# Kernel tuning notes

Hardware: AMD Instinct MI355X
Metric: run time of the kernel (lower is better)

## Reference

```python
import jax, jax.numpy as jnp
import numpy as np

EPS = 1e-5

def _conv(x, w, pad, groups=1):
    return jax.lax.conv_general_dilated(
        x, w, window_strides=(1, 1), padding=[(pad, pad), (pad, pad)],
        dimension_numbers=('NCHW', 'OIHW', 'NCHW'), feature_group_count=groups)

def _bn(x, g, b, m, v):
    # inference batch-norm, per-channel
    s = g * jax.lax.rsqrt(v + EPS)
    return x * s[None, :, None, None] + (b - m * s)[None, :, None, None]

def setup_inputs() -> dict:
    key = jax.random.key(0)
    ks = jax.random.split(key, 20)
    B, C, H, W = 32, 128, 64, 64
    cs = C // 2  # c_split = 64
    d = {
        'x': jax.random.normal(ks[0], (B, C, H, W), jnp.float32),
        'weights': jax.random.uniform(ks[1], (B, 2), jnp.float32),
        'indices': jax.random.randint(ks[2], (B, 2), 0, 4, jnp.int32),
        # expert 0: Conv(cs -> C, k=3, p=1) + BN + SiLU
        'e0_w': jax.random.normal(ks[3], (C, cs, 3, 3), jnp.float32) * 0.05,
        'e0_g': jax.random.uniform(ks[4], (C,), jnp.float32, 0.5, 1.5),
        'e0_b': jax.random.normal(ks[5], (C,), jnp.float32) * 0.1,
        'e0_m': jax.random.normal(ks[6], (C,), jnp.float32) * 0.1,
        'e0_v': jax.random.uniform(ks[7], (C,), jnp.float32, 0.5, 1.5),
        # expert 1: depthwise 5x5 (cs, groups=cs) -> 1x1 (cs -> C) -> BN -> SiLU
        'e1_dw': jax.random.normal(ks[8], (cs, 1, 5, 5), jnp.float32) * 0.05,
        'e1_pw': jax.random.normal(ks[9], (C, cs, 1, 1), jnp.float32) * 0.05,
        'e1_g': jax.random.uniform(ks[10], (C,), jnp.float32, 0.5, 1.5),
        'e1_b': jax.random.normal(ks[11], (C,), jnp.float32) * 0.1,
        'e1_m': jax.random.normal(ks[12], (C,), jnp.float32) * 0.1,
        'e1_v': jax.random.uniform(ks[13], (C,), jnp.float32, 0.5, 1.5),
        # expert 2: GhostConv(C -> C): cv1 = Conv(C, C//2, 3), cv2 = Conv(C//2, C//2, 5, groups=C//2)
        'e2a_w': jax.random.normal(ks[14], (cs, C, 3, 3), jnp.float32) * 0.05,
        'e2a_g': jax.random.uniform(ks[15], (cs,), jnp.float32, 0.5, 1.5),
        'e2a_b': jax.random.normal(ks[16], (cs,), jnp.float32) * 0.1,
        'e2a_m': jax.random.normal(ks[17], (cs,), jnp.float32) * 0.1,
        'e2a_v': jax.random.uniform(ks[18], (cs,), jnp.float32, 0.5, 1.5),
        'e2b_w': jax.random.normal(ks[19], (cs, 1, 5, 5), jnp.float32) * 0.05,
    }
    ks2 = jax.random.split(jax.random.key(1), 4)
    d['e2b_g'] = jax.random.uniform(ks2[0], (cs,), jnp.float32, 0.5, 1.5)
    d['e2b_b'] = jax.random.normal(ks2[1], (cs,), jnp.float32) * 0.1
    d['e2b_m'] = jax.random.normal(ks2[2], (cs,), jnp.float32) * 0.1
    d['e2b_v'] = jax.random.uniform(ks2[3], (cs,), jnp.float32, 0.5, 1.5)
    return d

def _forward(x, weights, indices,
             e0_w, e0_g, e0_b, e0_m, e0_v,
             e1_dw, e1_pw, e1_g, e1_b, e1_m, e1_v,
             e2a_w, e2a_g, e2a_b, e2a_m, e2a_v,
             e2b_w, e2b_g, e2b_b, e2b_m, e2b_v):
    C = x.shape[1]
    cs = C // 2
    x_rgb, x_ir = x[:, :cs], x[:, cs:]
    # expert outputs computed densely over the whole batch, masked combine below
    e0 = jax.nn.silu(_bn(_conv(x_rgb, e0_w, pad=1), e0_g, e0_b, e0_m, e0_v))
    e1 = jax.nn.silu(_bn(_conv(_conv(x_ir, e1_dw, pad=2, groups=cs), e1_pw, pad=0),
                         e1_g, e1_b, e1_m, e1_v))
    g1 = jax.nn.silu(_bn(_conv(x, e2a_w, pad=1), e2a_g, e2a_b, e2a_m, e2a_v))
    g2 = jax.nn.silu(_bn(_conv(g1, e2b_w, pad=2, groups=cs), e2b_g, e2b_b, e2b_m, e2b_v))
    e2 = jnp.concatenate([g1, g2], axis=1)
    out = jnp.zeros_like(x)
    K = indices.shape[1]
    for k in range(K):  # small fixed top-k loop
        idx = indices[:, k][:, None, None, None]          # [B,1,1,1]
        w = weights[:, k][:, None, None, None]            # [B,1,1,1]
        out = out + jnp.where(idx == 0, e0 * w, 0.0)
        out = out + jnp.where(idx == 1, e1 * w, 0.0)
        out = out + jnp.where(idx == 2, e2 * w, 0.0)
        out = out + jnp.where(idx == 3, x * 0.1, 0.0)
    return out

def reference(x, weights, indices,
              e0_w, e0_g, e0_b, e0_m, e0_v,
              e1_dw, e1_pw, e1_g, e1_b, e1_m, e1_v,
              e2a_w, e2a_g, e2a_b, e2a_m, e2a_v,
              e2b_w, e2b_g, e2b_b, e2b_m, e2b_v):
    return _forward(x, weights, indices,
                    e0_w, e0_g, e0_b, e0_m, e0_v,
                    e1_dw, e1_pw, e1_g, e1_b, e1_m, e1_v,
                    e2a_w, e2a_g, e2a_b, e2a_m, e2a_v,
                    e2b_w, e2b_g, e2b_b, e2b_m, e2b_v)
```

## Files before the change

kernel.cpp:

```cpp
#include <hip/hip_runtime.h>

#define B_  32
#define C_  128
#define CS  64
#define H_  64
#define W_  64
#define HW  (H_*W_)

typedef __attribute__((ext_vector_type(8))) short bf16x8_t;
typedef __attribute__((ext_vector_type(4))) float f32x4_t;
typedef unsigned short u16;
typedef unsigned int   u32;

__device__ __forceinline__ float silu_f(float v) { return v / (1.f + __expf(-v)); }

__device__ __forceinline__ u16 f2bf(float f) {
    u32 u = __float_as_uint(f);
    u = (u + 0x7FFFu + ((u >> 16) & 1u)) >> 16;
    return (u16)u;
}
__device__ __forceinline__ float bf2f(u16 u) {
    return __uint_as_float(((u32)u) << 16);
}
__device__ __forceinline__ u32 cvtpk(float a, float b) {
    u32 r;
    asm("v_cvt_pk_bf16_f32 %0, %1, %2" : "=v"(r) : "v"(a), "v"(b));
    return r;
}

__device__ __forceinline__ void get_coeffs(const float* __restrict__ wts,
                                           const int* __restrict__ idxs, int b,
                                           float& c0, float& c1, float& c2, float& cid) {
    int   i0 = idxs[b*2+0], i1 = idxs[b*2+1];
    float w0 = wts[b*2+0],  w1 = wts[b*2+1];
    c0  = (i0==0?w0:0.f)   + (i1==0?w1:0.f);
    c1  = (i0==1?w0:0.f)   + (i1==1?w1:0.f);
    c2  = (i0==2?w0:0.f)   + (i1==2?w1:0.f);
    cid = (i0==3?0.1f:0.f) + (i1==3?0.1f:0.f);
}

__global__ __launch_bounds__(256) void k_prep(
    const float* __restrict__ e0w, const float* __restrict__ e2aw, const float* __restrict__ e1pw,
    u16* __restrict__ Wt0f, u16* __restrict__ Wt2f, u16* __restrict__ Wt1f)
{
    const int i0 = blockIdx.x*256 + threadIdx.x, stride = gridDim.x*256;
    for (int i = i0; i < 73728; i += stride) {
        int j = i&7, lane = (i>>3)&63, cog = (i>>9)&7, kc = (i>>12)&1, tap = i>>13;
        int co = cog*16 + (lane&15), ci = kc*32 + (lane>>4)*8 + j;
        Wt0f[i] = f2bf(e0w[(size_t)(co*64 + ci)*9 + tap]);
    }
    for (int i = i0; i < 73728; i += stride) {
        int j = i&7, lane = (i>>3)&63, cog = (i>>9)&3, kc = (i>>11)&3, tap = i>>13;
        int co = cog*16 + (lane&15), ci = kc*32 + (lane>>4)*8 + j;
        Wt2f[i] = f2bf(e2aw[(size_t)(co*128 + ci)*9 + tap]);
    }
    for (int i = i0; i < 8192; i += stride) {
        int j = i&7, lane = (i>>3)&63, cog = (i>>9)&7, kc = (i>>12)&1;
        int co = cog*16 + (lane&15), ci = kc*32 + (lane>>4)*8 + j;
        Wt1f[i] = f2bf(e1pw[(size_t)co*64 + ci]);
    }
}

__device__ __forceinline__ void stage_x(
    const float* __restrict__ xb,
    char* lin, int orow0, int t)
{
    f32x4_t V0[8], V1[8];
    #pragma unroll
    for (int k = 0; k < 8; ++k) {
        const int u = t + k*256;
        const int quad = u & 15, r = (u >> 4) & 3, cp = u >> 6;
        const int hh = orow0 - 1 + r;
        const int hcl = (hh < 0) ? 0 : ((hh > 63) ? 63 : hh);
        const float* p0 = xb + (size_t)(2*cp)*HW + hcl*64 + quad*4;
        asm volatile("global_load_dwordx4 %0, %1, off" : "=v"(V0[k]) : "v"(p0));
        asm volatile("global_load_dwordx4 %0, %1, off" : "=v"(V1[k]) : "v"(p0 + HW));
    }
    asm volatile("s_waitcnt vmcnt(0)" ::: "memory");
    __builtin_amdgcn_sched_barrier(0);
    #pragma unroll
    for (int k = 0; k < 8; ++k) {
        const int u = t + k*256;
        const int quad = u & 15, r = (u >> 4) & 3, cp = u >> 6;
        const int hh = orow0 - 1 + r;
        const bool ok = (hh >= 0 && hh < H_);
        #pragma unroll
        for (int j = 0; j < 4; ++j) {
            const int p = r*66 + quad*4 + j + 1;
            const u32 a = ((u32)p*128 + (u32)cp*4) ^ (((u32)(p & 7)) << 4);
            float f0 = ok ? V0[k][j] : 0.f;
            float f1 = ok ? V1[k][j] : 0.f;
            *(u32*)(lin + a) = cvtpk(f0, f1);
        }
    }
    {
        const int cp = t & 31, side = (t >> 5) & 1, r = t >> 6;
        const int p = r*66 + side*65;
        const u32 a = ((u32)p*128 + (u32)cp*4) ^ (((u32)(p & 7)) << 4);
        *(u32*)(lin + a) = 0u;
    }
}

template<int NCF, int NPF, int TK, int COUT>
__device__ __forceinline__ void conv_pass(
    const char* lin, const u16* __restrict__ wb, int koff,
    int rbase, int pxbase, int l15, int kg,
    f32x4_t (&acc)[NCF][NPF])
{
    bf16x8_t A0[NCF], A1[NCF], A2[NCF];

    auto issueA = [&](int i, bf16x8_t (&dst)[NCF]) {
        const int tap = i >> 1, kcl = i & 1;
        const u16* wt = wb + (size_t)((tap*TK + koff + kcl)*(COUT/16))*512;
        #pragma unroll
        for (int cf = 0; cf < NCF; ++cf)
            asm volatile("global_load_dwordx4 %0, %1, off"
                         : "=v"(dst[cf]) : "v"(wt + ((size_t)cf << 9)));
    };
    auto ldsB = [&](int i, int pf) -> bf16x8_t {
        const int tap = i >> 1, kcl = i & 1;
        const int dh = tap / 3, dwp = tap % 3;
        const int p = (rbase + dh)*66 + pxbase + pf*16 + l15 + dwp;
        u32 a = (u32)p*128 + (u32)kcl*64 + (u32)kg*16;
        a ^= ((u32)(p & 7)) << 4;
        return *(const bf16x8_t*)(lin + a);
    };

    issueA(0, A0);
    issueA(1, A1);
    #pragma unroll
    for (int i = 0; i < 18; ++i) {
        if (i + 2 < 18) {
            const int s = (i + 2) % 3;
            if (s == 0)      issueA(i + 2, A0);
            else if (s == 1) issueA(i + 2, A1);
            else             issueA(i + 2, A2);
        }
        if (i < 16)       asm volatile("s_waitcnt vmcnt(8)" ::: "memory");
        else if (i == 16) asm volatile("s_waitcnt vmcnt(4)" ::: "memory");
        else              asm volatile("s_waitcnt vmcnt(0)" ::: "memory");
        __builtin_amdgcn_sched_barrier(0);
        bf16x8_t* ac = (i % 3 == 0) ? A0 : ((i % 3 == 1) ? A1 : A2);
        #pragma unroll
        for (int pf = 0; pf < NPF; ++pf) {
            bf16x8_t bfr = ldsB(i, pf);
            #pragma unroll
            for (int cf = 0; cf < NCF; ++cf)
                acc[cf][pf] = __builtin_amdgcn_mfma_f32_16x16x32_bf16(ac[cf], bfr, acc[cf][pf], 0, 0, 0);
        }
    }
}

__global__ __launch_bounds__(256, 3) void k_conv(
    const float* __restrict__ x,
    const float* __restrict__ wts, const int* __restrict__ idxs,
    const u16* __restrict__ Wt0f, const u16* __restrict__ Wt2f,
    const float* __restrict__ e0g, const float* __restrict__ e0b,
    const float* __restrict__ e0m, const float* __restrict__ e0v,
    const float* __restrict__ e2ag, const float* __restrict__ e2ab,
    const float* __restrict__ e2am, const float* __restrict__ e2av,
    const float* __restrict__ e1dw, const u16* __restrict__ Wt1f,
    const float* __restrict__ e1g, const float* __restrict__ e1b,
    const float* __restrict__ e1m, const float* __restrict__ e1v,
    float* __restrict__ out, u16* __restrict__ g1)
{
    __shared__ char uni[33792];
    const int b = blockIdx.y, orow0 = blockIdx.x*2, t = threadIdx.x;
    float c0, c1, c2, cid;
    get_coeffs(wts, idxs, b, c0, c1, c2, cid);

    const int lane = t & 63, l15 = lane & 15, kg = lane >> 4, wv = t >> 6;
    const float* xb = x + (size_t)b*C_*HW;

    if (blockIdx.z == 1) {
        if (c2 == 0.f) return;

        const int rw = wv >> 1, pw = wv & 1;
        const int pxbase = pw*32;
        f32x4_t acc[4][2];
        #pragma unroll
        for (int cf = 0; cf < 4; ++cf)
            #pragma unroll
            for (int pf = 0; pf < 2; ++pf)
                acc[cf][pf] = (f32x4_t){0.f, 0.f, 0.f, 0.f};

        const u16* wb = Wt2f + (size_t)lane*8;

        stage_x(xb, uni, orow0, t);
        __syncthreads();
        conv_pass<4, 2, 4, 64>(uni, wb, 0, rw, pxbase, l15, kg, acc);
        __syncthreads();
        stage_x(xb + (size_t)CS*HW, uni, orow0, t);
        __syncthreads();
        conv_pass<4, 2, 4, 64>(uni, wb, 2, rw, pxbase, l15, kg, acc);

        #pragma unroll
        for (int cf = 0; cf < 4; ++cf) {
            float sarr[4], tarr[4];
            #pragma unroll
            for (int r = 0; r < 4; ++r) {
                int co = cf*16 + kg*4 + r;
                float s = e2ag[co] * rsqrtf(e2av[co] + 1e-5f);
                sarr[r] = s; tarr[r] = e2ab[co] - e2am[co]*s;
            }
            #pragma unroll
            for (int pf = 0; pf < 2; ++pf) {
                size_t rowoff = (size_t)(orow0 + rw)*64 + pxbase + pf*16 + l15;
                #pragma unroll
                for (int r = 0; r < 4; ++r) {
                    int co = cf*16 + kg*4 + r;
                    float v = silu_f(acc[cf][pf][r]*sarr[r] + tarr[r]);
                    g1[((size_t)(b*CS+co))*HW + rowoff] = f2bf(v);
                }
            }
        }
        return;
    }

    const int cw = wv >> 1, rw = wv & 1;
    const int cobase = cw*64;

    if (c0 != 0.f) {
        stage_x(xb, uni, orow0, t);
        __syncthreads();

        f32x4_t acc[4][4];
        #pragma unroll
        for (int cf = 0; cf < 4; ++cf)
            #pragma unroll
            for (int pf = 0; pf < 4; ++pf)
                acc[cf][pf] = (f32x4_t){0.f, 0.f, 0.f, 0.f};

        const u16* wb = Wt0f + (size_t)(cobase >> 4)*512 + (size_t)lane*8;
        conv_pass<4, 4, 2, 128>(uni, wb, 0, rw, 0, l15, kg, acc);

        #pragma unroll
        for (int cf = 0; cf < 4; ++cf) {
            float sarr[4], tarr[4];
            #pragma unroll
            for (int r = 0; r < 4; ++r) {
                int co = cobase + cf*16 + kg*4 + r;
                float s = e0g[co] * rsqrtf(e0v[co] + 1e-5f);
                sarr[r] = s; tarr[r] = e0b[co] - e0m[co]*s;
            }
            #pragma unroll
            for (int pf = 0; pf < 4; ++pf) {
                size_t rowoff = (size_t)(orow0 + rw)*64 + pf*16 + l15;
                #pragma unroll
                for (int r = 0; r < 4; ++r) {
                    int co = cobase + cf*16 + kg*4 + r;
                    float v = silu_f(acc[cf][pf][r]*sarr[r] + tarr[r]);
                    size_t o = ((size_t)(b*C_+co))*HW + rowoff;
                    float idv = (cid != 0.f) ? cid*x[o] : 0.f;
                    out[o] = c0*v + idv;
                }
            }
        }
    } else if (c1 == 0.f) {
        for (int i = t; i < 4096; i += 256) {
            int ch = i >> 5, q = i & 31;
            size_t o = ((size_t)(b*C_+ch))*HW + (size_t)orow0*64 + q*4;
            float4 ov;
            if (cid != 0.f) {
                float4 xv = *(const float4*)(x + o);
                ov.x = cid*xv.x; ov.y = cid*xv.y; ov.z = cid*xv.z; ov.w = cid*xv.w;
            } else { ov.x = ov.y = ov.z = ov.w = 0.f; }
            *(float4*)(out + o) = ov;
        }
        return;
    } else {
        #pragma unroll
        for (int cf = 0; cf < 4; ++cf)
            #pragma unroll
            for (int pf = 0; pf < 4; ++pf) {
                size_t rowoff = (size_t)(orow0 + rw)*64 + pf*16 + l15;
                #pragma unroll
                for (int r = 0; r < 4; ++r) {
                    int co = cobase + cf*16 + kg*4 + r;
                    size_t o = ((size_t)(b*C_+co))*HW + rowoff;
                    out[o] = (cid != 0.f) ? cid*x[o] : 0.f;
                }
            }
    }

    if (c1 == 0.f) return;

    u16*   lin4 = (u16*)uni;
    u16*   lout = (u16*)(uni + 13440);
    float* wlf  = (float*)(uni + 31872);

    __syncthreads();

    #pragma unroll
    for (int pass = 0; pass < 4; ++pass) {
        if (pass) __syncthreads();
        for (int i = t; i < 6*16*16; i += 256) {
            int q = i & 15, chs = (i >> 4) & 15, r = i >> 8;
            int hh = orow0 - 2 + r;
            u32 w0 = 0u, w1 = 0u;
            if (hh >= 0 && hh < H_) {
                float4 v = *(const float4*)(x + ((size_t)(b*C_ + CS + pass*16 + chs))*HW + hh*64 + q*4);
                w0 = cvtpk(v.x, v.y); w1 = cvtpk(v.z, v.w);
            }
            u32* dst = (u32*)&lin4[(r*16 + chs)*70 + 2 + q*4];
            dst[0] = w0; dst[1] = w1;
        }
        for (int i = t; i < 6*16; i += 256) {
            int chs = i & 15, r = i >> 4;
            *(u32*)&lin4[(r*16 + chs)*70] = 0u;
            u32* e = (u32*)&lin4[(r*16 + chs)*70 + 66];
            e[0] = 0u; e[1] = 0u;
        }
        for (int i = t; i < 16*25; i += 256)
            wlf[(i/25)*26 + (i%25)] = e1dw[pass*16*25 + i];
        __syncthreads();

        {
            const int outrow = wv & 1, pxhalf = wv >> 1;
            const int chloc = l15;
            const int px0 = pxhalf*32 + kg*8;
            const float* wch = &wlf[chloc*26];
            float accp[8];
            #pragma unroll
            for (int p = 0; p < 8; ++p) accp[p] = 0.f;
            #pragma unroll
            for (int kh = 0; kh < 5; ++kh) {
                const u16* src = &lin4[((outrow + kh)*16 + chloc)*70 + px0];
                float rb[12];
                #pragma unroll
                for (int k = 0; k < 6; ++k) {
                    u32 u = *(const u32*)(src + 2*k);
                    rb[2*k]   = __uint_as_float(u << 16);
                    rb[2*k+1] = __uint_as_float(u & 0xFFFF0000u);
                }
                #pragma unroll
                for (int kw = 0; kw < 5; ++kw) {
                    float wvv = wch[kh*5 + kw];
                    #pragma unroll
                    for (int p = 0; p < 8; ++p) accp[p] += rb[p+kw]*wvv;
                }
            }
            #pragma unroll
            for (int p = 0; p < 8; ++p)
                lout[(outrow*64 + px0 + p)*72 + pass*16 + chloc] = f2bf(accp[p]);
        }
    }
    __syncthreads();

    {
        const int pwv = rw;
        f32x4_t acc1[4][4];
        #pragma unroll
        for (int cf = 0; cf < 4; ++cf)
            #pragma unroll
            for (int pf = 0; pf < 4; ++pf)
                acc1[cf][pf] = (f32x4_t){0.f, 0.f, 0.f, 0.f};

        #pragma unroll
        for (int kc = 0; kc < 2; ++kc) {
            const u16* wt = Wt1f + (((size_t)(kc*8 + cw*4)) << 9) + lane*8;
            bf16x8_t af[4];
            #pragma unroll
            for (int cf = 0; cf < 4; ++cf) af[cf] = *(const bf16x8_t*)(wt + (cf << 9));
            const int k0 = kc*32 + kg*8;
            #pragma unroll
            for (int pf = 0; pf < 4; ++pf) {
                bf16x8_t bfr = *(const bf16x8_t*)&lout[(pwv*64 + pf*16 + l15)*72 + k0];
                #pragma unroll
                for (int cf = 0; cf < 4; ++cf)
                    acc1[cf][pf] = __builtin_amdgcn_mfma_f32_16x16x32_bf16(af[cf], bfr, acc1[cf][pf], 0, 0, 0);
            }
        }

        #pragma unroll
        for (int cf = 0; cf < 4; ++cf) {
            float sarr[4], tarr[4];
            #pragma unroll
            for (int r = 0; r < 4; ++r) {
                int co = cw*64 + cf*16 + kg*4 + r;
                float s = e1g[co] * rsqrtf(e1v[co] + 1e-5f);
                sarr[r] = s; tarr[r] = e1b[co] - e1m[co]*s;
            }
            #pragma unroll
            for (int pf = 0; pf < 4; ++pf) {
                size_t rowoff = (size_t)(orow0 + pwv)*64 + pf*16 + l15;
                #pragma unroll
                for (int r = 0; r < 4; ++r) {
                    int co = cw*64 + cf*16 + kg*4 + r;
                    float v = silu_f(acc1[cf][pf][r]*sarr[r] + tarr[r]);
                    out[((size_t)(b*C_+co))*HW + rowoff] += c1*v;
                }
            }
        }
    }
}

__global__ __launch_bounds__(256) void k_e2b(
    const u16* __restrict__ g1, const float* __restrict__ wts, const int* __restrict__ idxs,
    const float* __restrict__ dww, const float* __restrict__ gg, const float* __restrict__ bb,
    const float* __restrict__ mm, const float* __restrict__ vv, float* __restrict__ out)
{
    const int b = blockIdx.y, band = blockIdx.x, t = threadIdx.x;
    const int orow0 = band*2;

    float c0, c1, c2, cid;
    get_coeffs(wts, idxs, b, c0, c1, c2, cid);
    if (c2 == 0.f) return;

    __shared__ u16  lin32[6*32*70];
    __shared__ float wl32[32*26];

    const int lane = t & 63, l15 = lane & 15, kg = lane >> 4;
    const int wv = t >> 6, outrow = wv & 1, cg = wv >> 1;

    #pragma unroll
    for (int pass = 0; pass < 2; ++pass) {
        if (pass) __syncthreads();
        for (int i = t; i < 6*32*16; i += 256) {
            int q = i & 15, chs = (i >> 4) & 31, r = i >> 9;
            int hh = orow0 - 2 + r;
            u32 w0 = 0u, w1 = 0u;
            if (hh >= 0 && hh < H_) {
                const u32* src = (const u32*)(g1 + ((size_t)(b*CS + pass*32 + chs))*HW + hh*64 + q*4);
                w0 = src[0]; w1 = src[1];
            }
            u32* dst = (u32*)&lin32[(r*32 + chs)*70 + 2 + q*4];
            dst[0] = w0; dst[1] = w1;
        }
        for (int i = t; i < 6*32; i += 256) {
            int chs = i & 31, r = i >> 5;
            *(u32*)&lin32[(r*32 + chs)*70] = 0u;
            u32* e = (u32*)&lin32[(r*32 + chs)*70 + 66];
            e[0] = 0u; e[1] = 0u;
        }
        for (int i = t; i < 32*25; i += 256)
            wl32[(i/25)*26 + (i%25)] = dww[pass*32*25 + i];
        __syncthreads();

        for (int i = t; i < 2*32*16; i += 256) {
            int q = i & 15, chs = (i >> 4) & 31, r = i >> 9;
            const u16* src = &lin32[((r+2)*32 + chs)*70 + 2 + q*4];
            float* op = out + ((size_t)(b*C_ + pass*32 + chs))*HW + (size_t)(orow0+r)*64 + q*4;
            float4 ov = *(float4*)op;
            ov.x += c2*bf2f(src[0]); ov.y += c2*bf2f(src[1]);
            ov.z += c2*bf2f(src[2]); ov.w += c2*bf2f(src[3]);
            *(float4*)op = ov;
        }

        {
            const int chloc = cg*16 + l15;
            const float* wch = &wl32[chloc*26];
            float accp[16];
            #pragma unroll
            for (int p = 0; p < 16; ++p) accp[p] = 0.f;
            #pragma unroll
            for (int kh = 0; kh < 5; ++kh) {
                const u16* src = &lin32[((outrow + kh)*32 + chloc)*70 + kg*16];
                float rb[20];
                #pragma unroll
                for (int k = 0; k < 10; ++k) {
                    u32 u = *(const u32*)(src + 2*k);
                    rb[2*k]   = __uint_as_float(u << 16);
                    rb[2*k+1] = __uint_as_float(u & 0xFFFF0000u);
                }
                #pragma unroll
                for (int kw = 0; kw < 5; ++kw) {
                    float wvv = wch[kh*5 + kw];
                    #pragma unroll
                    for (int p = 0; p < 16; ++p) accp[p] += rb[p+kw]*wvv;
                }
            }
            const int chg = pass*32 + chloc;
            float s = gg[chg] * rsqrtf(vv[chg] + 1e-5f);
            float tt = bb[chg] - mm[chg]*s;
            float* op = out + ((size_t)(b*C_ + CS + chg))*HW + (size_t)(orow0+outrow)*64 + kg*16;
            #pragma unroll
            for (int q = 0; q < 4; ++q) {
                float4 ov = *(float4*)(op + q*4);
                ov.x += c2*silu_f(accp[q*4+0]*s + tt);
                ov.y += c2*silu_f(accp[q*4+1]*s + tt);
                ov.z += c2*silu_f(accp[q*4+2]*s + tt);
                ov.w += c2*silu_f(accp[q*4+3]*s + tt);
                *(float4*)(op + q*4) = ov;
            }
        }
    }
}

extern "C" void kernel_launch(void* const* d_in, const int* in_sizes, int n_in,
                              void* d_out, int out_size, void* d_ws, size_t ws_size,
                              hipStream_t stream) {
    const float* x    = (const float*)d_in[0];
    const float* wts  = (const float*)d_in[1];
    const int*   idxs = (const int*)  d_in[2];
    const float* e0w  = (const float*)d_in[3];
    const float* e0g  = (const float*)d_in[4];
    const float* e0b  = (const float*)d_in[5];
    const float* e0m  = (const float*)d_in[6];
    const float* e0v  = (const float*)d_in[7];
    const float* e1dw = (const float*)d_in[8];
    const float* e1pw = (const float*)d_in[9];
    const float* e1g  = (const float*)d_in[10];
    const float* e1b  = (const float*)d_in[11];
    const float* e1m  = (const float*)d_in[12];
    const float* e1v  = (const float*)d_in[13];
    const float* e2aw = (const float*)d_in[14];
    const float* e2ag = (const float*)d_in[15];
    const float* e2ab = (const float*)d_in[16];
    const float* e2am = (const float*)d_in[17];
    const float* e2av = (const float*)d_in[18];
    const float* e2bw = (const float*)d_in[19];
    const float* e2bg = (const float*)d_in[20];
    const float* e2bb = (const float*)d_in[21];
    const float* e2bm = (const float*)d_in[22];
    const float* e2bv = (const float*)d_in[23];

    float* out = (float*)d_out;

    u16* g1   = (u16*)d_ws;
    u16* Wt0f = g1 + (size_t)8388608;
    u16* Wt2f = Wt0f + 73728;
    u16* Wt1f = Wt2f + 73728;

    k_prep<<<128, 256, 0, stream>>>(e0w, e2aw, e1pw, Wt0f, Wt2f, Wt1f);
    k_conv<<<dim3(32, B_, 2), 256, 0, stream>>>(
        x, wts, idxs, Wt0f, Wt2f,
        e0g, e0b, e0m, e0v, e2ag, e2ab, e2am, e2av,
        e1dw, Wt1f, e1g, e1b, e1m, e1v, out, g1);
    k_e2b<<<dim3(32, B_), 256, 0, stream>>>(
        g1, wts, idxs, e2bw, e2bg, e2bb, e2bm, e2bv, out);
}
```

Measured before the change: 94.49 us.

## Build compacted work list of active expert tiles and launch flat grid

k_prep now builds a compacted work list of (type, batch, band) items. Only tiles whose expert is active are included, ordered so the heavy GhostConv (e2a) tiles come first, then e0 tiles, then e1-only and identity-only tiles. k_conv launches a flat 2048-block grid and each block reads its item, so blocks for inactive experts exit immediately instead of being scheduled through the old 3D grid. Heavier work is also front-loaded for better load balance. This costs a serial single-thread list build in k_prep and an extra global read per block.

Result: slower. 116.6 us (+23.4%).

```diff
diff --git a/kernel.cpp b/kernel.cpp
--- a/kernel.cpp
+++ b/kernel.cpp
@@ -41,7 +41,9 @@
 
 __global__ __launch_bounds__(256) void k_prep(
     const float* __restrict__ e0w, const float* __restrict__ e2aw, const float* __restrict__ e1pw,
-    u16* __restrict__ Wt0f, u16* __restrict__ Wt2f, u16* __restrict__ Wt1f)
+    const float* __restrict__ wts, const int* __restrict__ idxs,
+    u16* __restrict__ Wt0f, u16* __restrict__ Wt2f, u16* __restrict__ Wt1f,
+    u32* __restrict__ wl)
 {
     const int i0 = blockIdx.x*256 + threadIdx.x, stride = gridDim.x*256;
     for (int i = i0; i < 73728; i += stride) {
@@ -58,6 +60,38 @@
         int j = i&7, lane = (i>>3)&63, cog = (i>>9)&7, kc = (i>>12)&1;
         int co = cog*16 + (lane&15), ci = kc*32 + (lane>>4)*8 + j;
         Wt1f[i] = f2bf(e1pw[(size_t)co*64 + ci]);
+    }
+
+    if (blockIdx.x == 0) {
+        __shared__ u32 base[4][32];
+        if (threadIdx.x == 0) {
+            u32 n = 0;
+            for (int tp = 0; tp < 4; ++tp) {
+                int tq = (tp == 0) ? 1 : (tp == 1) ? 0 : tp;
+                for (int bb = 0; bb < 32; ++bb) {
+                    float c0, c1, c2, cid;
+                    get_coeffs(wts, idxs, bb, c0, c1, c2, cid);
+                    bool act =
+                        (tq == 1) ? (c2 != 0.f) :
+                        (tq == 0) ? (c0 != 0.f) :
+                        (tq == 2) ? (c0 == 0.f && c1 != 0.f) :
+                                    (c0 == 0.f && c1 == 0.f);
+                    base[tq][bb] = act ? n : 0xFFFFFFFFu;
+                    if (act) n += 32;
+                }
+            }
+            wl[0] = n;
+        }
+        __syncthreads();
+        if (threadIdx.x < 32) {
+            for (int tq = 0; tq < 4; ++tq)
+                for (int bb = 0; bb < 32; ++bb) {
+                    u32 bs = base[tq][bb];
+                    if (bs != 0xFFFFFFFFu)
+                        wl[1 + bs + threadIdx.x] =
+                            ((u32)tq << 10) | ((u32)bb << 5) | (u32)threadIdx.x;
+                }
+        }
     }
 }
 
@@ -162,19 +196,23 @@
     const float* __restrict__ e1dw, const u16* __restrict__ Wt1f,
     const float* __restrict__ e1g, const float* __restrict__ e1b,
     const float* __restrict__ e1m, const float* __restrict__ e1v,
-    float* __restrict__ out, u16* __restrict__ g1)
+    float* __restrict__ out, u16* __restrict__ g1, const u32* __restrict__ wl)
 {
     __shared__ char uni[33792];
-    const int b = blockIdx.y, orow0 = blockIdx.x*2, t = threadIdx.x;
+    const int t = threadIdx.x;
+    const u32 n = wl[0];
+    if (blockIdx.x >= n) return;
+    const u32 item = wl[1 + blockIdx.x];
+    const int tp = item >> 10, b = (item >> 5) & 31, band = item & 31;
+    const int orow0 = band*2;
+
     float c0, c1, c2, cid;
     get_coeffs(wts, idxs, b, c0, c1, c2, cid);
 
     const int lane = t & 63, l15 = lane & 15, kg = lane >> 4, wv = t >> 6;
     const float* xb = x + (size_t)b*C_*HW;
 
-    if (blockIdx.z == 1) {
-        if (c2 == 0.f) return;
-
+    if (tp == 1) {
         const int rw = wv >> 1, pw = wv & 1;
         const int pxbase = pw*32;
         f32x4_t acc[4][2];
@@ -217,46 +255,7 @@
         return;
     }
 
-    const int cw = wv >> 1, rw = wv & 1;
-    const int cobase = cw*64;
-
-    if (c0 != 0.f) {
-        stage_x(xb, uni, orow0, t);
-        __syncthreads();
-
-        f32x4_t acc[4][4];
-        #pragma unroll
-        for (int cf = 0; cf < 4; ++cf)
-            #pragma unroll
-            for (int pf = 0; pf < 4; ++pf)
-                acc[cf][pf] = (f32x4_t){0.f, 0.f, 0.f, 0.f};
-
-        const u16* wb = Wt0f + (size_t)(cobase >> 4)*512 + (size_t)lane*8;
-        conv_pass<4, 4, 2, 128>(uni, wb, 0, rw, 0, l15, kg, acc);
-
-        #pragma unroll
-        for (int cf = 0; cf < 4; ++cf) {
-            float sarr[4], tarr[4];
-            #pragma unroll
-            for (int r = 0; r < 4; ++r) {
-                int co = cobase + cf*16 + kg*4 + r;
-                float s = e0g[co] * rsqrtf(e0v[co] + 1e-5f);
-                sarr[r] = s; tarr[r] = e0b[co] - e0m[co]*s;
-            }
-            #pragma unroll
-            for (int pf = 0; pf < 4; ++pf) {
-                size_t rowoff = (size_t)(orow0 + rw)*64 + pf*16 + l15;
-                #pragma unroll
-                for (int r = 0; r < 4; ++r) {
-                    int co = cobase + cf*16 + kg*4 + r;
-                    float v = silu_f(acc[cf][pf][r]*sarr[r] + tarr[r]);
-                    size_t o = ((size_t)(b*C_+co))*HW + rowoff;
-                    float idv = (cid != 0.f) ? cid*x[o] : 0.f;
-                    out[o] = c0*v + idv;
-                }
-            }
-        }
-    } else if (c1 == 0.f) {
+    if (tp == 3) {
         for (int i = t; i < 4096; i += 256) {
             int ch = i >> 5, q = i & 31;
             size_t o = ((size_t)(b*C_+ch))*HW + (size_t)orow0*64 + q*4;
@@ -268,6 +267,48 @@
             *(float4*)(out + o) = ov;
         }
         return;
+    }
+
+    const int cw = wv >> 1, rw = wv & 1;
+    const int cobase = cw*64;
+
+    if (tp == 0) {
+        stage_x(xb, uni, orow0, t);
+        __syncthreads();
+
+        f32x4_t acc[4][4];
+        #pragma unroll
+        for (int cf = 0; cf < 4; ++cf)
+            #pragma unroll
+            for (int pf = 0; pf < 4; ++pf)
+                acc[cf][pf] = (f32x4_t){0.f, 0.f, 0.f, 0.f};
+
+        const u16* wb = Wt0f + (size_t)(cobase >> 4)*512 + (size_t)lane*8;
+        conv_pass<4, 4, 2, 128>(uni, wb, 0, rw, 0, l15, kg, acc);
+
+        #pragma unroll
+        for (int cf = 0; cf < 4; ++cf) {
+            float sarr[4], tarr[4];
+            #pragma unroll
+            for (int r = 0; r < 4; ++r) {
+                int co = cobase + cf*16 + kg*4 + r;
+                float s = e0g[co] * rsqrtf(e0v[co] + 1e-5f);
+                sarr[r] = s; tarr[r] = e0b[co] - e0m[co]*s;
+            }
+            #pragma unroll
+            for (int pf = 0; pf < 4; ++pf) {
+                size_t rowoff = (size_t)(orow0 + rw)*64 + pf*16 + l15;
+                #pragma unroll
+                for (int r = 0; r < 4; ++r) {
+                    int co = cobase + cf*16 + kg*4 + r;
+                    float v = silu_f(acc[cf][pf][r]*sarr[r] + tarr[r]);
+                    size_t o = ((size_t)(b*C_+co))*HW + rowoff;
+                    float idv = (cid != 0.f) ? cid*x[o] : 0.f;
+                    out[o] = c0*v + idv;
+                }
+            }
+        }
+        if (c1 == 0.f) return;
     } else {
         #pragma unroll
         for (int cf = 0; cf < 4; ++cf)
@@ -282,8 +323,6 @@
                 }
             }
     }
-
-    if (c1 == 0.f) return;
 
     u16*   lin4 = (u16*)uni;
     u16*   lout = (u16*)(uni + 13440);
@@ -521,12 +560,13 @@
     u16* Wt0f = g1 + (size_t)8388608;
     u16* Wt2f = Wt0f + 73728;
     u16* Wt1f = Wt2f + 73728;
-
-    k_prep<<<128, 256, 0, stream>>>(e0w, e2aw, e1pw, Wt0f, Wt2f, Wt1f);
-    k_conv<<<dim3(32, B_, 2), 256, 0, stream>>>(
+    u32* wl   = (u32*)(Wt1f + 8192);
+
+    k_prep<<<128, 256, 0, stream>>>(e0w, e2aw, e1pw, wts, idxs, Wt0f, Wt2f, Wt1f, wl);
+    k_conv<<<2048, 256, 0, stream>>>(
         x, wts, idxs, Wt0f, Wt2f,
         e0g, e0b, e0m, e0v, e2ag, e2ab, e2am, e2av,
-        e1dw, Wt1f, e1g, e1b, e1m, e1v, out, g1);
+        e1dw, Wt1f, e1g, e1b, e1m, e1v, out, g1, wl);
     k_e2b<<<dim3(32, B_), 256, 0, stream>>>(
         g1, wts, idxs, e2bw, e2bg, e2bb, e2bm, e2bv, out);
 }
```
